# Performance work log

Measured on AMD Instinct MI355X. Metric: run time of the kernel, lower is better.

The kernel has to match this reference:

```python
import jax, jax.numpy as jnp
import numpy as np

N, E, IN_DIM, HID, NUM_CLASSES = 100000, 1600000, 256, 128, 40


def setup_inputs() -> dict:
    key = jax.random.key(0)
    ks = jax.random.split(key, 16)
    f32 = jnp.float32

    def w(k, shape):
        fan_in = shape[0]
        return (jax.random.normal(k, shape, f32) / jnp.sqrt(jnp.asarray(fan_in, f32)))

    x = jax.random.normal(ks[0], (N, IN_DIM), f32)
    edge_index = jax.random.randint(ks[1], (2, E), 0, N, dtype=jnp.int32)
    adj_embed = jax.random.normal(ks[2], (N, HID), f32) * 0.02  # xavier-ish
    return {
        "x": x,
        "edge_index": edge_index,
        "adj_embed": adj_embed,
        "wx1": w(ks[3], (IN_DIM, HID)), "bx1": jnp.zeros((HID,), f32),
        "wx2": w(ks[4], (HID, HID)),    "bx2": jnp.zeros((HID,), f32),
        "wa1": w(ks[5], (HID, HID)),    "ba1": jnp.zeros((HID,), f32),
        "wa2": w(ks[6], (HID, HID)),    "ba2": jnp.zeros((HID,), f32),
        "ww1": w(ks[7], (2 * HID, HID)), "bw1": jnp.zeros((HID,), f32),
        "wc": w(ks[8], (HID, NUM_CLASSES)), "bc": jnp.zeros((NUM_CLASSES,), f32),
    }


def _aggregate_neighbours(edge_index, weights, num_nodes):
    src, dst = edge_index[0], edge_index[1]
    # scatter-sum of gathered rows [E, HID] into [num_nodes, HID]
    agg = jax.ops.segment_sum(weights[src], dst, num_segments=num_nodes)
    deg = jax.ops.segment_sum(jnp.ones_like(dst, dtype=weights.dtype), dst,
                              num_segments=num_nodes)
    deg = jnp.maximum(deg, 1.0)[:, None]
    return agg / deg


def reference(x, edge_index, adj_embed, wx1, bx1, wx2, bx2,
              wa1, ba1, wa2, ba2, ww1, bw1, wc, bc):
    # mlp_x (dropout = identity in eval mode)
    hx = jax.nn.relu(x @ wx1 + bx1) @ wx2 + bx2          # [N, HID]
    # adjacency branch: mean-aggregate learned node embeddings over edges
    ha_raw = _aggregate_neighbours(edge_index, adj_embed, adj_embed.shape[0])
    ha = jax.nn.relu(ha_raw @ wa1 + ba1) @ wa2 + ba2     # [N, HID]
    # mlp_w over concat (num_layers=1 -> single Linear+ReLU)
    combined = jnp.concatenate([hx, ha], axis=1)         # [N, 2*HID]
    h = jax.nn.relu(combined @ ww1 + bw1)                # [N, HID]
    h = jax.nn.relu(h + hx + ha)
    logits = h @ wc + bc                                 # [N, NUM_CLASSES]
    return logits
```

## Files before the change

kernel.cpp:

```cpp
#include <hip/hip_runtime.h>

#define Nn 100000
#define Ee 1600000
#define IND 256
#define HD 128
#define NCLS 40
#define NBLK 391

typedef _Float16 f16;
typedef f16 f16x8 __attribute__((ext_vector_type(8)));
typedef float f32x4 __attribute__((ext_vector_type(4)));

#define INIT_ACC(BIAS)                                                    \
    _Pragma("unroll")                                                     \
    for (int q = 0; q < 4; q++) {                                         \
        float bv = (BIAS)[(fh * 4 + q) * 16 + (lane & 15)];               \
        acc[q][0] = bv; acc[q][1] = bv; acc[q][2] = bv; acc[q][3] = bv;   \
    }

#define GEMM_K128(APACK, BP)                                                  \
    _Pragma("unroll")                                                         \
    for (int kt = 0; kt < 4; kt++) {                                          \
        f16x8 a = *(const f16x8*)((APACK) + ((mt * 4 + kt) * 64 + lane) * 8); \
        _Pragma("unroll")                                                     \
        for (int q = 0; q < 4; q++) {                                         \
            f16x8 b = *(const f16x8*)((BP) + (((fh*4+q)*4 + kt)*64 + lane)*8);\
            acc[q] = __builtin_amdgcn_mfma_f32_16x16x32_f16(a, b, acc[q], 0, 0, 0); \
        }                                                                     \
    }

#define EPILOGUE(MODE, PDST)                                                  \
    _Pragma("unroll")                                                         \
    for (int q = 0; q < 4; q++) {                                             \
        int f = (fh * 4 + q) * 16 + (lane & 15);                              \
        int kt2 = f >> 5, q2 = (f >> 3) & 3, j2 = f & 7;                      \
        _Pragma("unroll")                                                     \
        for (int r = 0; r < 4; r++) {                                         \
            int n = (lane >> 4) * 4 + r;                                      \
            float v = acc[q][r];                                              \
            if (MODE == 0) v = fmaxf(v, 0.f);                                 \
            if (MODE == 2) rreg[q][r] += v;                                   \
            if (MODE == 3) v = fmaxf(fmaxf(v, 0.f) + rreg[q][r], 0.f);        \
            (PDST)[((mt * 4 + kt2) * 64 + n + 16 * q2) * 8 + j2] = (f16)v;    \
        }                                                                     \
    }

extern "C" __global__ void __launch_bounds__(256)
k_wpack(const float* __restrict__ wx1, const float* __restrict__ wx2,
        const float* __restrict__ wa1, const float* __restrict__ wa2,
        const float* __restrict__ ww1, const float* __restrict__ wc,
        f16* __restrict__ wp) {
    int idx = blockIdx.x * 256 + threadIdx.x;
    const float* W;
    int K, base;
    if (idx < 32768)       { W = wx1; K = 256; base = 0; }
    else if (idx < 49152)  { W = wx2; K = 128; base = 32768; }
    else if (idx < 65536)  { W = wa1; K = 128; base = 49152; }
    else if (idx < 81920)  { W = wa2; K = 128; base = 65536; }
    else if (idx < 114688) { W = ww1; K = 256; base = 81920; }
    else {
        int local = idx - 114688;
        int j = local & 7;
        int L = (local >> 3) & 63;
        int kt = (local >> 9) & 3;
        int ft = local / 2048;
        int k = kt * 32 + (L >> 4) * 8 + j;
        int n = ft * 16 + (L & 15);
        wp[idx] = (n < NCLS) ? (f16)wc[k * NCLS + n] : (f16)0.f;
        return;
    }
    int local = idx - base;
    int KT = K >> 5;
    int j = local & 7;
    int L = (local >> 3) & 63;
    int kt = (local >> 9) % KT;
    int ft = local / (512 * KT);
    int k = kt * 32 + (L >> 4) * 8 + j;
    int n = ft * 16 + (L & 15);
    wp[idx] = (f16)W[k * HD + n];
}

extern "C" __global__
__attribute__((amdgpu_flat_work_group_size(256, 256), amdgpu_waves_per_eu(4, 4)))
void k_prep(const int* __restrict__ ei, int* __restrict__ counts,
            int* __restrict__ rank,
            const float* __restrict__ emb, f16* __restrict__ embh,
            const float* __restrict__ x,
            const f16* __restrict__ wx1p, const float* __restrict__ bx1,
            const f16* __restrict__ wx2p, const float* __restrict__ bx2,
            f16* __restrict__ hxp) {
    __shared__ __align__(16) f16 pshr[4096];
    int bid = blockIdx.x;
    int t = threadIdx.x;

    int kind, p;
    if (bid < 10934) {
        int g = bid / 7, r = bid - g * 7;
        if (r == 0)      { kind = 0; p = g; }
        else if (r <= 4) { kind = 1; p = g * 4 + (r - 1); }
        else             { kind = 2; p = g * 2 + (r - 5); }
    } else {
        int r = bid - 10934;
        if (r == 0)      { kind = 0; p = 1562; }
        else if (r <= 2) { kind = 1; p = 6248 + (r - 1); }
        else             { kind = 2; p = 3124; }
    }

    if (kind == 0) {
        int e0 = p * 1024 + t;
#pragma unroll
        for (int k = 0; k < 4; k++) {
            int e = e0 + k * 256;
            if (e < Ee) {
                int dst = ei[Ee + e];
                rank[e] = atomicAdd(&counts[dst], 1);
            }
        }
        return;
    }
    if (kind == 1) {
        int i = p * 256 + t;
        const float4* pp = (const float4*)emb + (size_t)i * 2;
        float4 a = pp[0], b = pp[1];
        f16x8 h;
        h[0] = (f16)a.x; h[1] = (f16)a.y; h[2] = (f16)a.z; h[3] = (f16)a.w;
        h[4] = (f16)b.x; h[5] = (f16)b.y; h[6] = (f16)b.z; h[7] = (f16)b.w;
        *(f16x8*)(embh + (size_t)i * 8) = h;
        return;
    }
    int unit = p;
    const int node0 = unit * 32;
    const int lane = t & 63;
    const int wid = t >> 6;
    const int mt = wid >> 1;
    const int fh = wid & 1;
    f32x4 acc[4];
    float rreg[4][4];
    (void)rreg;

    INIT_ACC(bx1)
    {
        const float* xbase = x + (size_t)(node0 + mt * 16 + (lane & 15)) * IND
                               + (lane >> 4) * 8;
        float4 u[16];
#pragma unroll
        for (int kt = 0; kt < 8; kt++) {
            u[2 * kt]     = *(const float4*)(xbase + kt * 32);
            u[2 * kt + 1] = *(const float4*)(xbase + kt * 32 + 4);
        }
#pragma unroll
        for (int kt = 0; kt < 8; kt++) {
            float4 u0 = u[2 * kt], u1 = u[2 * kt + 1];
            f16x8 a;
            a[0] = (f16)u0.x; a[1] = (f16)u0.y; a[2] = (f16)u0.z; a[3] = (f16)u0.w;
            a[4] = (f16)u1.x; a[5] = (f16)u1.y; a[6] = (f16)u1.z; a[7] = (f16)u1.w;
#pragma unroll
            for (int q = 0; q < 4; q++) {
                f16x8 b = *(const f16x8*)(wx1p + (((fh*4+q)*8 + kt)*64 + lane)*8);
                acc[q] = __builtin_amdgcn_mfma_f32_16x16x32_f16(a, b, acc[q], 0, 0, 0);
            }
        }
    }
    EPILOGUE(0, pshr)
    __syncthreads();

    INIT_ACC(bx2)
    GEMM_K128(pshr, wx2p)
    {
        int gnt = unit * 2 + mt;
#pragma unroll
        for (int q = 0; q < 4; q++) {
            int f = (fh * 4 + q) * 16 + (lane & 15);
            int kt2 = f >> 5, q2 = (f >> 3) & 3, j2 = f & 7;
#pragma unroll
            for (int r = 0; r < 4; r++) {
                int n = (lane >> 4) * 4 + r;
                hxp[((gnt * 4 + kt2) * 64 + n + 16 * q2) * 8 + j2] = (f16)acc[q][r];
            }
        }
    }
}

extern "C" __global__ void __launch_bounds__(256)
k_scan1(const int* __restrict__ counts, int* __restrict__ bsum) {
    __shared__ int s[256];
    int t = threadIdx.x;
    int i = blockIdx.x * 256 + t;
    s[t] = (i < Nn) ? counts[i] : 0;
    __syncthreads();
    for (int d = 128; d > 0; d >>= 1) {
        if (t < d) s[t] += s[t + d];
        __syncthreads();
    }
    if (t == 0) bsum[blockIdx.x] = s[0];
}

extern "C" __global__ void __launch_bounds__(256)
k_scan3(const int* __restrict__ counts, const int* __restrict__ bsum,
        int* __restrict__ offsets) {
    __shared__ int s[256];
    __shared__ int basev;
    int t = threadIdx.x;
    int i = blockIdx.x * 256 + t;
    int partial = 0;
    for (int k = t; k < blockIdx.x; k += 256) partial += bsum[k];
    s[t] = partial;
    __syncthreads();
    for (int d = 128; d > 0; d >>= 1) {
        if (t < d) s[t] += s[t + d];
        __syncthreads();
    }
    if (t == 0) basev = s[0];
    __syncthreads();
    int v = (i < Nn) ? counts[i] : 0;
    s[t] = v;
    __syncthreads();
    for (int d = 1; d < 256; d <<= 1) {
        int x = (t >= d) ? s[t - d] : 0;
        __syncthreads();
        s[t] += x;
        __syncthreads();
    }
    if (i < Nn) offsets[i] = basev + s[t] - v;
    if (i == 0) offsets[Nn] = Ee;
}

extern "C" __global__ void __launch_bounds__(256)
k_scatter2(const int* __restrict__ ei, const int* __restrict__ offsets,
           const int* __restrict__ rank, int* __restrict__ bucket) {
    int e = blockIdx.x * 256 + threadIdx.x;
    int dst = ei[Ee + e];
    __builtin_nontemporal_store(ei[e], &bucket[offsets[dst] + rank[e]]);
}

extern "C" __global__ void __launch_bounds__(256)
k_gather(const int* __restrict__ offsets, const int* __restrict__ bucket,
         const f16* __restrict__ embh, f16* __restrict__ harawp) {
    int t = threadIdx.x;
    int lane = t & 63;
    int node = blockIdx.x * 4 + (t >> 6);
    int q = lane >> 4;
    int cl = (lane & 15) * 8;

    int beg = offsets[node];
    int end = offsets[node + 1];
    int deg = end - beg;

    int myidx = (lane < deg) ? bucket[beg + lane] : 0;

    float s[8];
#pragma unroll
    for (int j = 0; j < 8; j++) s[j] = 0.f;

    int dlim = (deg < 64) ? deg : 64;
    int e = q;
    for (; e + 4 < dlim; e += 8) {
        int a0 = __shfl(myidx, e);
        int a1 = __shfl(myidx, e + 4);
        f16x8 v0 = *(const f16x8*)(embh + (size_t)a0 * HD + cl);
        f16x8 v1 = *(const f16x8*)(embh + (size_t)a1 * HD + cl);
#pragma unroll
        for (int j = 0; j < 8; j++) s[j] += (float)v0[j] + (float)v1[j];
    }
    if (e < dlim) {
        int a0 = __shfl(myidx, e);
        f16x8 v0 = *(const f16x8*)(embh + (size_t)a0 * HD + cl);
#pragma unroll
        for (int j = 0; j < 8; j++) s[j] += (float)v0[j];
    }
    for (int i = beg + 64 + q; i < end; i += 4) {
        int a0 = bucket[i];
        f16x8 v0 = *(const f16x8*)(embh + (size_t)a0 * HD + cl);
#pragma unroll
        for (int j = 0; j < 8; j++) s[j] += (float)v0[j];
    }

#pragma unroll
    for (int j = 0; j < 8; j++) {
        s[j] += __shfl_down(s[j], 32);
        s[j] += __shfl_down(s[j], 16);
    }

    if (lane < 16) {
        float inv = 1.0f / fmaxf((float)deg, 1.0f);
        f16x8 h;
#pragma unroll
        for (int j = 0; j < 8; j++) h[j] = (f16)(s[j] * inv);
        int nt = node >> 4, m = node & 15;
        int kt = lane >> 2, q2 = lane & 3;
        *(f16x8*)(harawp + (((nt * 4 + kt) * 64 + m + 16 * q2) * 8)) = h;
    }
}

extern "C" __global__ void __launch_bounds__(256, 4)
linkx_mlp(const f16* __restrict__ harawp, const f16* __restrict__ hxp,
          const f16* __restrict__ wa1p, const float* __restrict__ ba1,
          const f16* __restrict__ wa2p, const float* __restrict__ ba2,
          const f16* __restrict__ ww1p, const float* __restrict__ bw1,
          const f16* __restrict__ wcp, const float* __restrict__ bc,
          float* __restrict__ out) {
    __shared__ __align__(16) f16 shr[4096];
    __shared__ __align__(16) f16 hap[4096];

    const int t = threadIdx.x;
    const int node0 = blockIdx.x * 32;
    const int lane = t & 63;
    const int wid = t >> 6;
    const int mt = wid >> 1;
    const int fh = wid & 1;
    const int gntb = (node0 >> 4) + mt;

    f32x4 acc[4];
    float rreg[4][4];

    f16 hxr[4][4];
#pragma unroll
    for (int q = 0; q < 4; q++) {
        int f = (fh * 4 + q) * 16 + (lane & 15);
        int kt2 = f >> 5, q2 = (f >> 3) & 3, j2 = f & 7;
#pragma unroll
        for (int r = 0; r < 4; r++) {
            int n = (lane >> 4) * 4 + r;
            hxr[q][r] = hxp[((gntb * 4 + kt2) * 64 + n + 16 * q2) * 8 + j2];
        }
    }

    INIT_ACC(ba1)
    {
        f16x8 av[4];
#pragma unroll
        for (int kt = 0; kt < 4; kt++)
            av[kt] = *(const f16x8*)(harawp + ((gntb * 4 + kt) * 64 + lane) * 8);
#pragma unroll
        for (int kt = 0; kt < 4; kt++) {
#pragma unroll
            for (int q = 0; q < 4; q++) {
                f16x8 b = *(const f16x8*)(wa1p + (((fh*4+q)*4 + kt)*64 + lane)*8);
                acc[q] = __builtin_amdgcn_mfma_f32_16x16x32_f16(av[kt], b, acc[q], 0, 0, 0);
            }
        }
    }
    EPILOGUE(0, shr)
    __syncthreads();

#pragma unroll
    for (int q = 0; q < 4; q++)
#pragma unroll
        for (int r = 0; r < 4; r++) rreg[q][r] = (float)hxr[q][r];

    INIT_ACC(ba2)
    GEMM_K128(shr, wa2p)
    EPILOGUE(2, hap)
    __syncthreads();

    INIT_ACC(bw1)
#pragma unroll
    for (int kt = 0; kt < 4; kt++) {
        f16x8 a = *(const f16x8*)(hxp + ((gntb * 4 + kt) * 64 + lane) * 8);
#pragma unroll
        for (int q = 0; q < 4; q++) {
            f16x8 b = *(const f16x8*)(ww1p + (((fh*4+q)*8 + kt)*64 + lane)*8);
            acc[q] = __builtin_amdgcn_mfma_f32_16x16x32_f16(a, b, acc[q], 0, 0, 0);
        }
    }
#pragma unroll
    for (int kt = 4; kt < 8; kt++) {
        f16x8 a = *(const f16x8*)(hap + ((mt * 4 + (kt - 4)) * 64 + lane) * 8);
#pragma unroll
        for (int q = 0; q < 4; q++) {
            f16x8 b = *(const f16x8*)(ww1p + (((fh*4+q)*8 + kt)*64 + lane)*8);
            acc[q] = __builtin_amdgcn_mfma_f32_16x16x32_f16(a, b, acc[q], 0, 0, 0);
        }
    }
    EPILOGUE(3, shr)
    __syncthreads();

    {
        int nft = (fh == 0) ? 2 : 1;
#pragma unroll 2
        for (int ii = 0; ii < nft; ii++) {
            int ft = (ii == 0) ? fh : 2;
            int f = ft * 16 + (lane & 15);
            f32x4 c;
            float bv = (f < NCLS) ? bc[f] : 0.f;
            c[0] = bv; c[1] = bv; c[2] = bv; c[3] = bv;
#pragma unroll
            for (int kt = 0; kt < 4; kt++) {
                f16x8 a = *(const f16x8*)(shr + ((mt * 4 + kt) * 64 + lane) * 8);
                f16x8 b = *(const f16x8*)(wcp + ((ft * 4 + kt) * 64 + lane) * 8);
                c = __builtin_amdgcn_mfma_f32_16x16x32_f16(a, b, c, 0, 0, 0);
            }
            if (f < NCLS) {
#pragma unroll
                for (int r = 0; r < 4; r++) {
                    int n = node0 + mt * 16 + (lane >> 4) * 4 + r;
                    out[(size_t)n * NCLS + f] = c[r];
                }
            }
        }
    }
}

extern "C" void kernel_launch(void* const* d_in, const int* in_sizes, int n_in,
                              void* d_out, int out_size, void* d_ws, size_t ws_size,
                              hipStream_t stream) {
    const float* x   = (const float*)d_in[0];
    const int*   ei  = (const int*)d_in[1];
    const float* emb = (const float*)d_in[2];
    const float* wx1 = (const float*)d_in[3];
    const float* bx1 = (const float*)d_in[4];
    const float* wx2 = (const float*)d_in[5];
    const float* bx2 = (const float*)d_in[6];
    const float* wa1 = (const float*)d_in[7];
    const float* ba1 = (const float*)d_in[8];
    const float* wa2 = (const float*)d_in[9];
    const float* ba2 = (const float*)d_in[10];
    const float* ww1 = (const float*)d_in[11];
    const float* bw1 = (const float*)d_in[12];
    const float* wc  = (const float*)d_in[13];
    const float* bc  = (const float*)d_in[14];
    float* out = (float*)d_out;

    int* ws = (int*)d_ws;
    int* counts  = ws;
    int* offsets = ws + 2 * Nn;
    int* bsum    = ws + 3 * Nn + 16;
    int* bucket  = ws + 3 * Nn + 512;
    f16* wp      = (f16*)(ws + 3 * Nn + 512 + Ee);
    f16* wx1p = wp;
    f16* wx2p = wp + 32768;
    f16* wa1p = wp + 49152;
    f16* wa2p = wp + 65536;
    f16* ww1p = wp + 81920;
    f16* wcp  = wp + 114688;
    f16* harawp = wp + 131072;
    f16* embh   = harawp + (size_t)Nn * HD;
    f16* hxp    = embh + (size_t)Nn * HD;
    int* rank = (int*)harawp;

    hipMemsetAsync(ws, 0, (size_t)Nn * sizeof(int), stream);

    k_wpack<<<472, 256, 0, stream>>>(wx1, wx2, wa1, wa2, ww1, wc, wp);
    k_prep<<<10938, 256, 0, stream>>>(ei, counts, rank, emb, embh,
                                      x, wx1p, bx1, wx2p, bx2, hxp);
    k_scan1<<<NBLK, 256, 0, stream>>>(counts, bsum);
    k_scan3<<<NBLK, 256, 0, stream>>>(counts, bsum, offsets);
    k_scatter2<<<Ee / 256, 256, 0, stream>>>(ei, offsets, rank, bucket);
    k_gather<<<Nn / 4, 256, 0, stream>>>(offsets, bucket, embh, harawp);

    linkx_mlp<<<Nn / 32, 256, 0, stream>>>(harawp, hxp,
                                           wa1p, ba1, wa2p, ba2,
                                           ww1p, bw1, wcp, bc, out);
}
```

Baseline: 440.2 us.

## Fuse neighbour gather-mean into MLP kernel via shared-memory staging

Removes the separate k_gather launch. Each MLP block now aggregates its own 32 nodes' neighbour embeddings into shared memory and feeds them straight to the first GEMM, so the haraw intermediate is no longer written to and read back from global memory. It also drops the prep kernel's waves-per-EU constraint, switches the scatter to a normal store, and raises the MLP occupancy hint to 5 blocks. The trade-off is a longer serial gather phase inside each MLP block, 8 nodes per wave, before any MFMA work starts, plus extra shared memory and register pressure.

Result: faster. 426.9 us (-3.0%).

```diff
diff --git a/kernel.cpp b/kernel.cpp
--- a/kernel.cpp
+++ b/kernel.cpp
@@ -80,15 +80,14 @@
     wp[idx] = (f16)W[k * HD + n];
 }
 
-extern "C" __global__
-__attribute__((amdgpu_flat_work_group_size(256, 256), amdgpu_waves_per_eu(4, 4)))
-void k_prep(const int* __restrict__ ei, int* __restrict__ counts,
-            int* __restrict__ rank,
-            const float* __restrict__ emb, f16* __restrict__ embh,
-            const float* __restrict__ x,
-            const f16* __restrict__ wx1p, const float* __restrict__ bx1,
-            const f16* __restrict__ wx2p, const float* __restrict__ bx2,
-            f16* __restrict__ hxp) {
+extern "C" __global__ void __launch_bounds__(256)
+k_prep(const int* __restrict__ ei, int* __restrict__ counts,
+       int* __restrict__ rank,
+       const float* __restrict__ emb, f16* __restrict__ embh,
+       const float* __restrict__ x,
+       const f16* __restrict__ wx1p, const float* __restrict__ bx1,
+       const f16* __restrict__ wx2p, const float* __restrict__ bx2,
+       f16* __restrict__ hxp) {
     __shared__ __align__(16) f16 pshr[4096];
     int bid = blockIdx.x;
     int t = threadIdx.x;
@@ -230,75 +229,18 @@
            const int* __restrict__ rank, int* __restrict__ bucket) {
     int e = blockIdx.x * 256 + threadIdx.x;
     int dst = ei[Ee + e];
-    __builtin_nontemporal_store(ei[e], &bucket[offsets[dst] + rank[e]]);
-}
-
-extern "C" __global__ void __launch_bounds__(256)
-k_gather(const int* __restrict__ offsets, const int* __restrict__ bucket,
-         const f16* __restrict__ embh, f16* __restrict__ harawp) {
-    int t = threadIdx.x;
-    int lane = t & 63;
-    int node = blockIdx.x * 4 + (t >> 6);
-    int q = lane >> 4;
-    int cl = (lane & 15) * 8;
-
-    int beg = offsets[node];
-    int end = offsets[node + 1];
-    int deg = end - beg;
-
-    int myidx = (lane < deg) ? bucket[beg + lane] : 0;
-
-    float s[8];
-#pragma unroll
-    for (int j = 0; j < 8; j++) s[j] = 0.f;
-
-    int dlim = (deg < 64) ? deg : 64;
-    int e = q;
-    for (; e + 4 < dlim; e += 8) {
-        int a0 = __shfl(myidx, e);
-        int a1 = __shfl(myidx, e + 4);
-        f16x8 v0 = *(const f16x8*)(embh + (size_t)a0 * HD + cl);
-        f16x8 v1 = *(const f16x8*)(embh + (size_t)a1 * HD + cl);
-#pragma unroll
-        for (int j = 0; j < 8; j++) s[j] += (float)v0[j] + (float)v1[j];
-    }
-    if (e < dlim) {
-        int a0 = __shfl(myidx, e);
-        f16x8 v0 = *(const f16x8*)(embh + (size_t)a0 * HD + cl);
-#pragma unroll
-        for (int j = 0; j < 8; j++) s[j] += (float)v0[j];
-    }
-    for (int i = beg + 64 + q; i < end; i += 4) {
-        int a0 = bucket[i];
-        f16x8 v0 = *(const f16x8*)(embh + (size_t)a0 * HD + cl);
-#pragma unroll
-        for (int j = 0; j < 8; j++) s[j] += (float)v0[j];
-    }
-
-#pragma unroll
-    for (int j = 0; j < 8; j++) {
-        s[j] += __shfl_down(s[j], 32);
-        s[j] += __shfl_down(s[j], 16);
-    }
-
-    if (lane < 16) {
-        float inv = 1.0f / fmaxf((float)deg, 1.0f);
-        f16x8 h;
-#pragma unroll
-        for (int j = 0; j < 8; j++) h[j] = (f16)(s[j] * inv);
-        int nt = node >> 4, m = node & 15;
-        int kt = lane >> 2, q2 = lane & 3;
-        *(f16x8*)(harawp + (((nt * 4 + kt) * 64 + m + 16 * q2) * 8)) = h;
-    }
-}
-
-extern "C" __global__ void __launch_bounds__(256, 4)
-linkx_mlp(const f16* __restrict__ harawp, const f16* __restrict__ hxp,
+    bucket[offsets[dst] + rank[e]] = ei[e];
+}
+
+extern "C" __global__ void __launch_bounds__(256, 5)
+linkx_mlp(const int* __restrict__ offsets, const int* __restrict__ bucket,
+          const f16* __restrict__ embh, const f16* __restrict__ hxp,
           const f16* __restrict__ wa1p, const float* __restrict__ ba1,
           const f16* __restrict__ wa2p, const float* __restrict__ ba2,
           const f16* __restrict__ ww1p, const float* __restrict__ bw1,
           const f16* __restrict__ wcp, const float* __restrict__ bc,
           float* __restrict__ out) {
+    __shared__ __align__(16) f16 hraw[4096];
     __shared__ __align__(16) f16 shr[4096];
     __shared__ __align__(16) f16 hap[4096];
 
@@ -310,6 +252,62 @@
     const int fh = wid & 1;
     const int gntb = (node0 >> 4) + mt;
 
+    {
+        int q = lane >> 4;
+        int cl = (lane & 15) * 8;
+#pragma unroll 1
+        for (int i = 0; i < 8; i++) {
+            int ln = wid * 8 + i;
+            int node = node0 + ln;
+            int beg = offsets[node];
+            int end = offsets[node + 1];
+            int deg = end - beg;
+            int myidx = (lane < deg) ? bucket[beg + lane] : 0;
+
+            float s[8];
+#pragma unroll
+            for (int j = 0; j < 8; j++) s[j] = 0.f;
+
+            int dlim = (deg < 64) ? deg : 64;
+            int e = q;
+            for (; e + 4 < dlim; e += 8) {
+                int a0 = __shfl(myidx, e);
+                int a1 = __shfl(myidx, e + 4);
+                f16x8 v0 = *(const f16x8*)(embh + (size_t)a0 * HD + cl);
+                f16x8 v1 = *(const f16x8*)(embh + (size_t)a1 * HD + cl);
+#pragma unroll
+                for (int j = 0; j < 8; j++) s[j] += (float)v0[j] + (float)v1[j];
+            }
+            if (e < dlim) {
+                int a0 = __shfl(myidx, e);
+                f16x8 v0 = *(const f16x8*)(embh + (size_t)a0 * HD + cl);
+#pragma unroll
+                for (int j = 0; j < 8; j++) s[j] += (float)v0[j];
+            }
+            for (int ii = beg + 64 + q; ii < end; ii += 4) {
+                int a0 = bucket[ii];
+                f16x8 v0 = *(const f16x8*)(embh + (size_t)a0 * HD + cl);
+#pragma unroll
+                for (int j = 0; j < 8; j++) s[j] += (float)v0[j];
+            }
+#pragma unroll
+            for (int j = 0; j < 8; j++) {
+                s[j] += __shfl_down(s[j], 32);
+                s[j] += __shfl_down(s[j], 16);
+            }
+            if (lane < 16) {
+                float inv = 1.0f / fmaxf((float)deg, 1.0f);
+                f16x8 h;
+#pragma unroll
+                for (int j = 0; j < 8; j++) h[j] = (f16)(s[j] * inv);
+                int lnt = ln >> 4, m = ln & 15;
+                int kt = lane >> 2, q2 = lane & 3;
+                *(f16x8*)(hraw + (((lnt * 4 + kt) * 64 + m + 16 * q2) * 8)) = h;
+            }
+        }
+    }
+    __syncthreads();
+
     f32x4 acc[4];
     float rreg[4][4];
 
@@ -326,20 +324,7 @@
     }
 
     INIT_ACC(ba1)
-    {
-        f16x8 av[4];
-#pragma unroll
-        for (int kt = 0; kt < 4; kt++)
-            av[kt] = *(const f16x8*)(harawp + ((gntb * 4 + kt) * 64 + lane) * 8);
-#pragma unroll
-        for (int kt = 0; kt < 4; kt++) {
-#pragma unroll
-            for (int q = 0; q < 4; q++) {
-                f16x8 b = *(const f16x8*)(wa1p + (((fh*4+q)*4 + kt)*64 + lane)*8);
-                acc[q] = __builtin_amdgcn_mfma_f32_16x16x32_f16(av[kt], b, acc[q], 0, 0, 0);
-            }
-        }
-    }
+    GEMM_K128(hraw, wa1p)
     EPILOGUE(0, shr)
     __syncthreads();
 
@@ -433,10 +418,9 @@
     f16* wa2p = wp + 65536;
     f16* ww1p = wp + 81920;
     f16* wcp  = wp + 114688;
-    f16* harawp = wp + 131072;
-    f16* embh   = harawp + (size_t)Nn * HD;
+    int* rank   = (int*)(wp + 131072);
+    f16* embh   = wp + 131072 + (size_t)Nn * HD;
     f16* hxp    = embh + (size_t)Nn * HD;
-    int* rank = (int*)harawp;
 
     hipMemsetAsync(ws, 0, (size_t)Nn * sizeof(int), stream);
 
@@ -446,9 +430,8 @@
     k_scan1<<<NBLK, 256, 0, stream>>>(counts, bsum);
     k_scan3<<<NBLK, 256, 0, stream>>>(counts, bsum, offsets);
     k_scatter2<<<Ee / 256, 256, 0, stream>>>(ei, offsets, rank, bucket);
-    k_gather<<<Nn / 4, 256, 0, stream>>>(offsets, bucket, embh, harawp);
-
-    linkx_mlp<<<Nn / 32, 256, 0, stream>>>(harawp, hxp,
+
+    linkx_mlp<<<Nn / 32, 256, 0, stream>>>(offsets, bucket, embh, hxp,
                                            wa1p, ba1, wa2p, ba2,
                                            ww1p, bw1, wcp, bc, out);
 }
```
